# Optimization experiments

Hardware: AMD Instinct MI355X
Metric: run time of the kernel (lower is better)

## Reference

```python
import jax, jax.numpy as jnp
import numpy as np

EPS_MSG = 1e-7
EPS_BN = 1e-5


def _seg_softmax(logits, seg, num_segments):
    # logits: [E, D] per-edge logits; softmax over edges sharing the same dst node
    m = jax.ops.segment_max(logits, seg, num_segments=num_segments)
    m = jnp.where(jnp.isfinite(m), m, 0.0)
    e = jnp.exp(logits - m[seg])
    s = jax.ops.segment_sum(e, seg, num_segments=num_segments)
    return e / (s[seg] + 1e-16)


def _batchnorm(h, gamma, beta):
    mu = jnp.mean(h, axis=0)
    var = jnp.var(h, axis=0)
    return (h - mu) * jax.lax.rsqrt(var + EPS_BN) * gamma + beta


def setup_inputs() -> dict:
    key = jax.random.key(0)
    ks = jax.random.split(key, 12)
    N, E, G, D, L = 100000, 600000, 512, 128, 7
    x = jax.random.randint(ks[0], (N, 9), 0, 64, dtype=jnp.int32)
    edge_index = jax.random.randint(ks[1], (2, E), 0, N, dtype=jnp.int32)
    edge_attr = jax.random.randint(ks[2], (E, 3), 0, 8, dtype=jnp.int32)
    batch = jnp.sort(jax.random.randint(ks[3], (N,), 0, G, dtype=jnp.int32))
    rf_pred = jax.random.uniform(ks[4], (G,), dtype=jnp.float32)
    atom_emb = jax.random.normal(ks[5], (9, 64, D), dtype=jnp.float32) * 0.02
    bond_emb = jax.random.normal(ks[6], (3, 8, D), dtype=jnp.float32) * 0.02
    conv_w = jax.random.normal(ks[7], (L, D, D), dtype=jnp.float32) * 0.02
    conv_b = jnp.zeros((L, D), dtype=jnp.float32)
    ts = jnp.ones((L,), dtype=jnp.float32)  # learnable inverse temperatures (init 1/t style)
    gammas = jnp.ones((L, D), dtype=jnp.float32)
    bn_betas = jnp.zeros((L, D), dtype=jnp.float32)
    final_w = jax.random.normal(ks[8], (D, 1), dtype=jnp.float32) * 0.02
    final_b = jnp.zeros((1,), dtype=jnp.float32)
    beta = jnp.array([0.5], dtype=jnp.float32)
    return {"x": x, "edge_index": edge_index, "edge_attr": edge_attr, "batch": batch,
            "rf_pred": rf_pred, "atom_emb": atom_emb, "bond_emb": bond_emb,
            "conv_w": conv_w, "conv_b": conv_b, "ts": ts, "gammas": gammas,
            "bn_betas": bn_betas, "final_w": final_w, "final_b": final_b, "beta": beta}


def reference(x, edge_index, edge_attr, batch, rf_pred, atom_emb, bond_emb,
              conv_w, conv_b, ts, gammas, bn_betas, final_w, final_b, beta):
    N = x.shape[0]
    G = rf_pred.shape[0]
    L = conv_w.shape[0]
    src, dst = edge_index[0], edge_index[1]

    # AtomEncoder / BondEncoder: sum of per-feature embeddings
    h = jax.vmap(lambda tab, idx: tab[idx], in_axes=(0, 1))(atom_emb, x).sum(0)          # [N, D]
    e_emb = jax.vmap(lambda tab, idx: tab[idx], in_axes=(0, 1))(bond_emb, edge_attr).sum(0)  # [E, D]

    def genconv(l, hin):
        msg = jax.nn.relu(hin[src] + e_emb) + EPS_MSG          # [E, D]
        alpha = _seg_softmax(msg * ts[l], dst, N)              # softmax aggregation weights
        aggr = jax.ops.segment_sum(alpha * msg, dst, num_segments=N)  # [N, D]
        return (hin + aggr) @ conv_w[l] + conv_b[l]

    # res+ DeeperGCN
    h = genconv(0, h)
    for l in range(1, L):
        h2 = jax.nn.relu(_batchnorm(h, gammas[l - 1], bn_betas[l - 1]))
        h = genconv(l, h2) + h
    h = jax.nn.relu(_batchnorm(h, gammas[L - 1], bn_betas[L - 1]))

    # mean graph pooling
    counts = jnp.maximum(jax.ops.segment_sum(jnp.ones((N,), h.dtype), batch, num_segments=G), 1.0)
    hg = jax.ops.segment_sum(h, batch, num_segments=G) / counts[:, None]  # [G, D]

    dgcn_pred = hg @ final_w + final_b  # [G, 1]
    return (1.0 - beta) * jax.nn.sigmoid(dgcn_pred) + beta * rf_pred.reshape(-1, 1)
```

## Files before the change

kernel.cpp:

```cpp
#include <hip/hip_runtime.h>
#include <hip/hip_fp16.h>
#include <math.h>

#define D 128
#define PF 8

typedef _Float16 f16x8 __attribute__((ext_vector_type(8)));
typedef float f32x4_t __attribute__((ext_vector_type(4)));


__global__ void hist_kernel(const int* __restrict__ edge_index, int* __restrict__ deg, int E) {
    int e = blockIdx.x * blockDim.x + threadIdx.x;
    if (e >= E) return;
    atomicAdd(&deg[edge_index[E + e]], 1);
}

__global__ void scanA_kernel(const int* __restrict__ deg, int* __restrict__ bsum, int n) {
    __shared__ int red[256];
    int b = blockIdx.x, t = threadIdx.x;
    int base = b * 1024 + t * 4;
    int s = 0;
#pragma unroll
    for (int j = 0; j < 4; ++j)
        if (base + j < n) s += deg[base + j];
    red[t] = s;
    __syncthreads();
    for (int off = 128; off > 0; off >>= 1) {
        if (t < off) red[t] += red[t + off];
        __syncthreads();
    }
    if (t == 0) bsum[b] = red[0];
}

__global__ void scanB_kernel(int* __restrict__ bsum, int nb) {
    __shared__ int sh[256];
    int t = threadIdx.x;
    sh[t] = (t < nb) ? bsum[t] : 0;
    __syncthreads();
    for (int off = 1; off < 256; off <<= 1) {
        int v = (t >= off) ? sh[t - off] : 0;
        __syncthreads();
        sh[t] += v;
        __syncthreads();
    }
    if (t < nb) bsum[t] = (t == 0) ? 0 : sh[t - 1];
}

__global__ void scanC_kernel(const int* __restrict__ deg, const int* __restrict__ boff,
                             int* __restrict__ row_start, int n) {
    __shared__ int sh[256];
    int b = blockIdx.x, t = threadIdx.x;
    int base = b * 1024 + t * 4;
    int v[4];
#pragma unroll
    for (int j = 0; j < 4; ++j) v[j] = (base + j < n) ? deg[base + j] : 0;
    int p[4];
    p[0] = 0; p[1] = v[0]; p[2] = v[0] + v[1]; p[3] = v[0] + v[1] + v[2];
    int s = p[3] + v[3];
    sh[t] = s;
    __syncthreads();
    for (int off = 1; off < 256; off <<= 1) {
        int x = (t >= off) ? sh[t - off] : 0;
        __syncthreads();
        sh[t] += x;
        __syncthreads();
    }
    int off0 = boff[b] + sh[t] - s;
#pragma unroll
    for (int j = 0; j < 4; ++j)
        if (base + j < n) row_start[base + j] = off0 + p[j];
    if (base <= n - 1 && n - 1 < base + 4) row_start[n] = off0 + s;
}

__global__ void scatter_kernel(const int* __restrict__ edge_index, const int* __restrict__ edge_attr,
                               int* __restrict__ cursor, int2* __restrict__ csr, int E) {
    int e = blockIdx.x * blockDim.x + threadIdx.x;
    if (e >= E) return;
    int src = edge_index[e];
    int dst = edge_index[E + e];
    int pos = atomicAdd(&cursor[dst], 1);
    int a0 = edge_attr[e * 3], a1 = edge_attr[e * 3 + 1], a2 = edge_attr[e * 3 + 2];
    csr[pos] = make_int2(src, a0 | (a1 << 3) | (a2 << 6));
}

__global__ void ev_build_kernel(const float* __restrict__ bond_emb, __half2* __restrict__ evt) {
    int idx = blockIdx.x * blockDim.x + threadIdx.x;
    if (idx >= 512 * 64) return;
    int combo = idx >> 6, j = idx & 63;
    int d0 = 2 * j;
    float ex = bond_emb[(combo & 7) * D + d0] +
               bond_emb[(8 + ((combo >> 3) & 7)) * D + d0] +
               bond_emb[(16 + ((combo >> 6) & 7)) * D + d0];
    float ey = bond_emb[(combo & 7) * D + d0 + 1] +
               bond_emb[(8 + ((combo >> 3) & 7)) * D + d0 + 1] +
               bond_emb[(16 + ((combo >> 6) & 7)) * D + d0 + 1];
    evt[idx] = __floats2half2_rn(ex, ey);
}

__global__ void wt_build_kernel(const float* __restrict__ conv_w, _Float16* __restrict__ wt,
                                int total) {
    int idx = blockIdx.x * blockDim.x + threadIdx.x;
    if (idx >= total) return;
    int l = idx >> 14;
    int rem = idx & 16383;
    int n = rem >> 7, k = rem & 127;
    wt[idx] = (_Float16)conv_w[(l << 14) + k * 128 + n];
}

__global__ void gstart_kernel(const int* __restrict__ batch, int* __restrict__ gstart,
                              int N, int G) {
    int n = blockIdx.x * blockDim.x + threadIdx.x;
    if (n >= N) return;
    if (n == 0) {
        for (int g = 0; g <= batch[0]; ++g) gstart[g] = 0;
    } else {
        int b0 = batch[n - 1], b1 = batch[n];
        for (int g = b0 + 1; g <= b1; ++g) gstart[g] = n;
    }
    if (n == N - 1) {
        for (int g = batch[N - 1] + 1; g <= G; ++g) gstart[g] = N;
    }
}


__global__ void atom_embed_kernel(const int* __restrict__ x,
                                  const float* __restrict__ atom_emb,
                                  _Float16* __restrict__ h16, int N) {
    long long idx = (long long)blockIdx.x * blockDim.x + threadIdx.x;
    if (idx >= (long long)N * D) return;
    int n = (int)(idx >> 7);
    int d = (int)(idx & 127);
    float acc = 0.f;
#pragma unroll
    for (int f = 0; f < 9; ++f) {
        int v = x[n * 9 + f];
        acc += atom_emb[(long long)(f * 64 + v) * D + d];
    }
    h16[idx] = (_Float16)acc;
}

__global__ void bn_reduce_finalize_kernel(const float* __restrict__ partial, int nb,
                                          const float* __restrict__ gamma,
                                          const float* __restrict__ bnbeta, float invN,
                                          float* __restrict__ aArr, float* __restrict__ bArr) {
    __shared__ float r1[256], r2[256];
    int d = blockIdx.x, t = threadIdx.x;
    float a1 = 0.f, a2 = 0.f;
    for (int i = t; i < nb; i += 256) {
        a1 += partial[(long long)i * 256 + d];
        a2 += partial[(long long)i * 256 + 128 + d];
    }
    r1[t] = a1; r2[t] = a2;
    __syncthreads();
    for (int off = 128; off > 0; off >>= 1) {
        if (t < off) { r1[t] += r1[t + off]; r2[t] += r2[t + off]; }
        __syncthreads();
    }
    if (t == 0) {
        float mean = r1[0] * invN;
        float var = r2[0] * invN - mean * mean;
        float a = rsqrtf(var + 1e-5f) * gamma[d];
        aArr[d] = a;
        bArr[d] = bnbeta[d] - mean * a;
    }
}

__global__ __launch_bounds__(128, 8) void fused_layer_kernel(
        const __half2* __restrict__ h16c,
        const float* __restrict__ aArr, const float* __restrict__ bArr, int applyBN,
        const float* __restrict__ ts, int l,
        const int* __restrict__ row_start, const int2* __restrict__ csr,
        const __half2* __restrict__ evt,
        const _Float16* __restrict__ wt, const float* __restrict__ bias,
        int residual, _Float16* __restrict__ h16out,
        float* __restrict__ partial, int N) {
    __shared__ __align__(16) char smem[8192];
    _Float16* yh = (_Float16*)smem;
    __half2* tile = (__half2*)smem;

    int t = threadIdx.x;
    int row0 = blockIdx.x * 16;
    int wave = t >> 6;
    int lane = t & 63;
    float tsl = ts[l];
    int a = row0 + wave * 8;

    float2 bnA = make_float2(1.f, 0.f), bnB = make_float2(0.f, 0.f);
    if (applyBN) {
        bnA = ((const float2*)aArr)[lane];
        bnB = ((const float2*)bArr)[lane];
    }

    int rsv = row_start[min(a + min(lane, 8), N)];
    int s0 = __builtin_amdgcn_readlane(rsv, 0);
    int s1 = __builtin_amdgcn_readlane(rsv, 8);

#pragma unroll
    for (int i = 0; i < 8; ++i) {
        int r = a + i;
        float2 hs = make_float2(0.f, 0.f);
        if (r < N) {
            hs = __half22float2(h16c[(size_t)r * 64 + lane]);
            if (applyBN) {
                hs.x = fmaxf(hs.x * bnA.x + bnB.x, 0.f);
                hs.y = fmaxf(hs.y * bnA.y + bnB.y, 0.f);
            }
        }
        tile[(wave * 8 + i) * 68 + lane] = __floats2half2_rn(hs.x, hs.y);
    }

    int c0 = s0;
    int2 ea = make_int2(0, 0);
    if (c0 + lane < s1) ea = csr[c0 + lane];

    __half2 hvS[PF], evS[PF];
#pragma unroll
    for (int k = 0; k < PF; ++k) {
        int pp = s0 + k;
        if (pp < s1) {
            int q = pp - c0;
            int srcp = __builtin_amdgcn_readlane(ea.x, q);
            int cbp = __builtin_amdgcn_readlane(ea.y, q);
            hvS[k] = h16c[(size_t)srcp * 64 + lane];
            evS[k] = evt[(size_t)cbp * 64 + lane];
        }
    }

    int cur = 0;
    int nend = __builtin_amdgcn_readlane(rsv, min(cur + 1, 8));
    while (cur < 8 && nend == s0) {
        cur++;
        nend = __builtin_amdgcn_readlane(rsv, min(cur + 1, 8));
    }

    float accwx = 0.f, accwy = 0.f, accmx = 0.f, accmy = 0.f;
    int total = s1 - s0;
    for (int it = 0; it < total; it += PF) {
#pragma unroll
        for (int k = 0; k < PF; ++k) {
            int p = s0 + it + k;
            if (p < s1) {
                float2 hv = __half22float2(hvS[k]);
                float2 ev = __half22float2(evS[k]);
                if (applyBN) {
                    hv.x = fmaxf(hv.x * bnA.x + bnB.x, 0.f);
                    hv.y = fmaxf(hv.y * bnA.y + bnB.y, 0.f);
                }
                float mx = fmaxf(hv.x + ev.x, 0.f) + 1e-7f;
                float my = fmaxf(hv.y + ev.y, 0.f) + 1e-7f;
                float wx = __expf(mx * tsl);
                float wy = __expf(my * tsl);
                accwx += wx; accmx += wx * mx;
                accwy += wy; accmy += wy * my;
                int pp = p + PF;
                if (pp < s1) {
                    if (pp >= c0 + 64) {
                        c0 += 64;
                        ea = (c0 + lane < s1) ? csr[c0 + lane] : make_int2(0, 0);
                    }
                    int q = pp - c0;
                    int srcp = __builtin_amdgcn_readlane(ea.x, q);
                    int cbp = __builtin_amdgcn_readlane(ea.y, q);
                    hvS[k] = h16c[(size_t)srcp * 64 + lane];
                    evS[k] = evt[(size_t)cbp * 64 + lane];
                }
                while (cur < 8 && nend == p + 1) {
                    int slot = (wave * 8 + cur) * 68 + lane;
                    float2 y = __half22float2(tile[slot]);
                    y.x += accmx / (accwx + 1e-16f);
                    y.y += accmy / (accwy + 1e-16f);
                    tile[slot] = __floats2half2_rn(y.x, y.y);
                    accwx = accwy = accmx = accmy = 0.f;
                    cur++;
                    nend = __builtin_amdgcn_readlane(rsv, min(cur + 1, 8));
                }
            }
        }
    }
    __syncthreads();

    int ln = t & 15;
    int quad = (t & 63) >> 4;
    const _Float16* h16in = (const _Float16*)h16c;

    float cs[4] = {0.f, 0.f, 0.f, 0.f};
    float cq[4] = {0.f, 0.f, 0.f, 0.f};
    const _Float16* ap = yh + ln * 136 + quad * 8;
#pragma unroll
    for (int ct = 0; ct < 4; ++ct) {
        int colg = (wave * 4 + ct) * 16 + ln;
        const _Float16* bp = wt + (size_t)colg * 128 + quad * 8;
        f32x4_t c = {0.f, 0.f, 0.f, 0.f};
#pragma unroll
        for (int kk = 0; kk < 4; ++kk) {
            f16x8 av = *(const f16x8*)(ap + kk * 32);
            f16x8 bv = *(const f16x8*)(bp + kk * 32);
            c = __builtin_amdgcn_mfma_f32_16x16x32_f16(av, bv, c, 0, 0, 0);
        }
        float bsv = bias[colg];
#pragma unroll
        for (int reg = 0; reg < 4; ++reg) {
            int r = row0 + quad * 4 + reg;
            if (r < N) {
                long long off = (long long)r * D + colg;
                float o = c[reg] + bsv;
                if (residual) o += (float)h16in[off];
                h16out[off] = (_Float16)o;
                cs[ct] += o; cq[ct] += o * o;
            }
        }
    }

    __syncthreads();
    float* stats = (float*)smem;
    int grp = wave * 4 + quad;
#pragma unroll
    for (int ct = 0; ct < 4; ++ct) {
        int colg = (wave * 4 + ct) * 16 + ln;
        stats[grp * 256 + colg] = cs[ct];
        stats[grp * 256 + 128 + colg] = cq[ct];
    }
    __syncthreads();
    float ssumA = 0.f, ssumB = 0.f;
#pragma unroll
    for (int g = 0; g < 8; ++g) {
        ssumA += stats[g * 256 + t];
        ssumB += stats[g * 256 + 128 + t];
    }
    partial[(long long)blockIdx.x * 256 + t] = ssumA;
    partial[(long long)blockIdx.x * 256 + 128 + t] = ssumB;
}

__global__ void pool_head_kernel(const _Float16* __restrict__ h16, const float* __restrict__ aArr,
                                 const float* __restrict__ bArr, const int* __restrict__ gstart,
                                 const float* __restrict__ fw, const float* __restrict__ fb,
                                 const float* __restrict__ beta, const float* __restrict__ rf,
                                 float* __restrict__ out) {
    __shared__ float red[256];
    int g = blockIdx.x, t = threadIdx.x;
    int d = t & 127, half = t >> 7;
    int s0 = gstart[g], s1 = gstart[g + 1];
    float a = aArr[d], b = bArr[d];
    float acc = 0.f;
    for (int n = s0 + half; n < s1; n += 2)
        acc += fmaxf((float)h16[(long long)n * D + d] * a + b, 0.f);
    red[t] = acc;
    __syncthreads();
    if (t < 128) red[t] += red[t + 128];
    __syncthreads();
    if (t < 64) {
        float v = red[t] * fw[t] + red[t + 64] * fw[t + 64];
#pragma unroll
        for (int off = 32; off > 0; off >>= 1) v += __shfl_down(v, off);
        if (t == 0) {
            float c = fmaxf((float)(s1 - s0), 1.f);
            float pred = v / c + fb[0];
            float sig = 1.f / (1.f + __expf(-pred));
            float bb = beta[0];
            out[g] = (1.f - bb) * sig + bb * rf[g];
        }
    }
}

static inline size_t align16(size_t x) { return (x + 15) & ~(size_t)15; }

extern "C" void kernel_launch(void* const* d_in, const int* in_sizes, int n_in,
                              void* d_out, int out_size, void* d_ws, size_t ws_size,
                              hipStream_t stream) {
    const int* x = (const int*)d_in[0];
    const int* edge_index = (const int*)d_in[1];
    const int* edge_attr = (const int*)d_in[2];
    const int* batch = (const int*)d_in[3];
    const float* rf_pred = (const float*)d_in[4];
    const float* atom_emb = (const float*)d_in[5];
    const float* bond_emb = (const float*)d_in[6];
    const float* conv_w = (const float*)d_in[7];
    const float* conv_b = (const float*)d_in[8];
    const float* ts = (const float*)d_in[9];
    const float* gammas = (const float*)d_in[10];
    const float* bn_betas = (const float*)d_in[11];
    const float* final_w = (const float*)d_in[12];
    const float* final_b = (const float*)d_in[13];
    const float* beta = (const float*)d_in[14];
    float* out = (float*)d_out;

    int N = in_sizes[0] / 9;
    int E = in_sizes[1] / 2;
    int G = in_sizes[4];
    int L = in_sizes[9];

    int mmBlocks = (N + 15) / 16;
    size_t ND = (size_t)N * D;

    char* p = (char*)d_ws;
    _Float16* h16_a = (_Float16*)p;  p += align16(ND * 2);
    _Float16* h16_b = (_Float16*)p;  p += align16(ND * 2);
    __half2* evt = (__half2*)p;      p += align16((size_t)512 * 64 * 4);
    _Float16* wt = (_Float16*)p;     p += align16((size_t)L * 16384 * 2);
    float* partial = (float*)p;      p += align16((size_t)256 * mmBlocks * 4);
    float* aArr = (float*)p;         p += align16((size_t)D * 4);
    float* bArr = (float*)p;         p += align16((size_t)D * 4);
    int* gstart = (int*)p;           p += align16((size_t)(G + 1) * 4);
    int* deg = (int*)p;              p += align16((size_t)N * 4);
    int* row_start = (int*)p;        p += align16((size_t)(N + 1) * 4);
    int* cursor = (int*)p;           p += align16((size_t)N * 4);
    int* bsum = (int*)p;             p += align16((size_t)256 * 4);
    int2* csr = (int2*)p;            p += align16((size_t)E * 8);

    long long ndThreads = (long long)N * D;
    int ndBlocks = (int)((ndThreads + 255) / 256);
    int eBlocks = (E + 255) / 256;
    int nBlocks = (N + 255) / 256;
    int nb1024 = (N + 1023) / 1024;
    int wtTotal = L * 16384;
    float invN = 1.0f / (float)N;

    hipMemsetAsync(deg, 0, (size_t)N * sizeof(int), stream);
    hist_kernel<<<eBlocks, 256, 0, stream>>>(edge_index, deg, E);
    scanA_kernel<<<nb1024, 256, 0, stream>>>(deg, bsum, N);
    scanB_kernel<<<1, 256, 0, stream>>>(bsum, nb1024);
    scanC_kernel<<<nb1024, 256, 0, stream>>>(deg, bsum, row_start, N);
    hipMemcpyAsync(cursor, row_start, (size_t)N * sizeof(int), hipMemcpyDeviceToDevice, stream);
    scatter_kernel<<<eBlocks, 256, 0, stream>>>(edge_index, edge_attr, cursor, csr, E);
    ev_build_kernel<<<(512 * 64 + 255) / 256, 256, 0, stream>>>(bond_emb, evt);
    wt_build_kernel<<<(wtTotal + 255) / 256, 256, 0, stream>>>(conv_w, wt, wtTotal);
    gstart_kernel<<<nBlocks, 256, 0, stream>>>(batch, gstart, N, G);

    atom_embed_kernel<<<ndBlocks, 256, 0, stream>>>(x, atom_emb, h16_a, N);

    _Float16* h16c = h16_a;
    _Float16* h16n = h16_b;
    for (int l = 0; l < L; ++l) {
        int applyBN = (l >= 1) ? 1 : 0;
        if (applyBN) {
            bn_reduce_finalize_kernel<<<128, 256, 0, stream>>>(
                partial, mmBlocks, gammas + (size_t)(l - 1) * D,
                bn_betas + (size_t)(l - 1) * D, invN, aArr, bArr);
        }
        fused_layer_kernel<<<mmBlocks, 128, 0, stream>>>(
            (const __half2*)h16c, aArr, bArr, applyBN, ts, l, row_start, csr, evt,
            wt + (size_t)l * 16384, conv_b + (size_t)l * D,
            applyBN, h16n, partial, N);
        _Float16* tmp16 = h16c; h16c = h16n; h16n = tmp16;
    }

    bn_reduce_finalize_kernel<<<128, 256, 0, stream>>>(
        partial, mmBlocks, gammas + (size_t)(L - 1) * D,
        bn_betas + (size_t)(L - 1) * D, invN, aArr, bArr);
    pool_head_kernel<<<G, 256, 0, stream>>>(h16c, aArr, bArr, gstart,
                                            final_w, final_b, beta, rf_pred, out);
}
```

Baseline: 917.8 us.

## Fuse setup kernels, prefetch CSR chunk, raise gather prefetch depth, register self rows

Merges the three small setup kernels into one launch and writes the cursor array inside the scan kernel instead of a separate device copy. In the fused layer kernel, self-row features are kept in registers and written to the LDS tile once per row close, avoiding a read-modify-write of the tile. The next 64-edge CSR chunk is now loaded ahead of time, and the gather prefetch depth goes from 8 to 12. This trades extra VGPR pressure, and possibly lower occupancy, for more memory-level parallelism.

```diff
diff --git a/kernel.cpp b/kernel.cpp
--- a/kernel.cpp
+++ b/kernel.cpp
@@ -3,7 +3,7 @@
 #include <math.h>
 
 #define D 128
-#define PF 8
+#define PF 12
 
 typedef _Float16 f16x8 __attribute__((ext_vector_type(8)));
 typedef float f32x4_t __attribute__((ext_vector_type(4)));
@@ -47,7 +47,7 @@
 }
 
 __global__ void scanC_kernel(const int* __restrict__ deg, const int* __restrict__ boff,
-                             int* __restrict__ row_start, int n) {
+                             int* __restrict__ row_start, int* __restrict__ cursor, int n) {
     __shared__ int sh[256];
     int b = blockIdx.x, t = threadIdx.x;
     int base = b * 1024 + t * 4;
@@ -68,7 +68,10 @@
     int off0 = boff[b] + sh[t] - s;
 #pragma unroll
     for (int j = 0; j < 4; ++j)
-        if (base + j < n) row_start[base + j] = off0 + p[j];
+        if (base + j < n) {
+            row_start[base + j] = off0 + p[j];
+            cursor[base + j] = off0 + p[j];
+        }
     if (base <= n - 1 && n - 1 < base + 4) row_start[n] = off0 + s;
 }
 
@@ -83,33 +86,32 @@
     csr[pos] = make_int2(src, a0 | (a1 << 3) | (a2 << 6));
 }
 
-__global__ void ev_build_kernel(const float* __restrict__ bond_emb, __half2* __restrict__ evt) {
+__global__ void misc_build_kernel(const float* __restrict__ bond_emb, __half2* __restrict__ evt,
+                                  const float* __restrict__ conv_w, _Float16* __restrict__ wt,
+                                  int wtTotal, const int* __restrict__ batch,
+                                  int* __restrict__ gstart, int N, int G) {
     int idx = blockIdx.x * blockDim.x + threadIdx.x;
-    if (idx >= 512 * 64) return;
-    int combo = idx >> 6, j = idx & 63;
-    int d0 = 2 * j;
-    float ex = bond_emb[(combo & 7) * D + d0] +
-               bond_emb[(8 + ((combo >> 3) & 7)) * D + d0] +
-               bond_emb[(16 + ((combo >> 6) & 7)) * D + d0];
-    float ey = bond_emb[(combo & 7) * D + d0 + 1] +
-               bond_emb[(8 + ((combo >> 3) & 7)) * D + d0 + 1] +
-               bond_emb[(16 + ((combo >> 6) & 7)) * D + d0 + 1];
-    evt[idx] = __floats2half2_rn(ex, ey);
-}
-
-__global__ void wt_build_kernel(const float* __restrict__ conv_w, _Float16* __restrict__ wt,
-                                int total) {
-    int idx = blockIdx.x * blockDim.x + threadIdx.x;
-    if (idx >= total) return;
-    int l = idx >> 14;
-    int rem = idx & 16383;
-    int n = rem >> 7, k = rem & 127;
-    wt[idx] = (_Float16)conv_w[(l << 14) + k * 128 + n];
-}
-
-__global__ void gstart_kernel(const int* __restrict__ batch, int* __restrict__ gstart,
-                              int N, int G) {
-    int n = blockIdx.x * blockDim.x + threadIdx.x;
+    if (idx < 512 * 64) {
+        int combo = idx >> 6, j = idx & 63;
+        int d0 = 2 * j;
+        float ex = bond_emb[(combo & 7) * D + d0] +
+                   bond_emb[(8 + ((combo >> 3) & 7)) * D + d0] +
+                   bond_emb[(16 + ((combo >> 6) & 7)) * D + d0];
+        float ey = bond_emb[(combo & 7) * D + d0 + 1] +
+                   bond_emb[(8 + ((combo >> 3) & 7)) * D + d0 + 1] +
+                   bond_emb[(16 + ((combo >> 6) & 7)) * D + d0 + 1];
+        evt[idx] = __floats2half2_rn(ex, ey);
+        return;
+    }
+    int widx = idx - 512 * 64;
+    if (widx < wtTotal) {
+        int l = widx >> 14;
+        int rem = widx & 16383;
+        int n = rem >> 7, k = rem & 127;
+        wt[widx] = (_Float16)conv_w[(l << 14) + k * 128 + n];
+        return;
+    }
+    int n = widx - wtTotal;
     if (n >= N) return;
     if (n == 0) {
         for (int g = 0; g <= batch[0]; ++g) gstart[g] = 0;
@@ -192,48 +194,71 @@
     }
 
     int rsv = row_start[min(a + min(lane, 8), N)];
+    __half2 zero2 = __floats2half2_rn(0.f, 0.f);
+    __half2 hsv0 = zero2, hsv1 = zero2, hsv2 = zero2, hsv3 = zero2;
+    __half2 hsv4 = zero2, hsv5 = zero2, hsv6 = zero2, hsv7 = zero2;
+    if (a + 0 < N) hsv0 = h16c[(size_t)(a + 0) * 64 + lane];
+    if (a + 1 < N) hsv1 = h16c[(size_t)(a + 1) * 64 + lane];
+    if (a + 2 < N) hsv2 = h16c[(size_t)(a + 2) * 64 + lane];
+    if (a + 3 < N) hsv3 = h16c[(size_t)(a + 3) * 64 + lane];
+    if (a + 4 < N) hsv4 = h16c[(size_t)(a + 4) * 64 + lane];
+    if (a + 5 < N) hsv5 = h16c[(size_t)(a + 5) * 64 + lane];
+    if (a + 6 < N) hsv6 = h16c[(size_t)(a + 6) * 64 + lane];
+    if (a + 7 < N) hsv7 = h16c[(size_t)(a + 7) * 64 + lane];
+
     int s0 = __builtin_amdgcn_readlane(rsv, 0);
     int s1 = __builtin_amdgcn_readlane(rsv, 8);
 
-#pragma unroll
-    for (int i = 0; i < 8; ++i) {
-        int r = a + i;
-        float2 hs = make_float2(0.f, 0.f);
-        if (r < N) {
-            hs = __half22float2(h16c[(size_t)r * 64 + lane]);
-            if (applyBN) {
-                hs.x = fmaxf(hs.x * bnA.x + bnB.x, 0.f);
-                hs.y = fmaxf(hs.y * bnA.y + bnB.y, 0.f);
-            }
-        }
-        tile[(wave * 8 + i) * 68 + lane] = __floats2half2_rn(hs.x, hs.y);
-    }
-
     int c0 = s0;
-    int2 ea = make_int2(0, 0);
-    if (c0 + lane < s1) ea = csr[c0 + lane];
+    int2 eaCur = make_int2(0, 0), eaNxt = make_int2(0, 0);
+    if (c0 + lane < s1) eaCur = csr[c0 + lane];
+    if (c0 + 64 + lane < s1) eaNxt = csr[c0 + 64 + lane];
 
     __half2 hvS[PF], evS[PF];
 #pragma unroll
     for (int k = 0; k < PF; ++k) {
         int pp = s0 + k;
         if (pp < s1) {
-            int q = pp - c0;
-            int srcp = __builtin_amdgcn_readlane(ea.x, q);
-            int cbp = __builtin_amdgcn_readlane(ea.y, q);
+            int srcp = __builtin_amdgcn_readlane(eaCur.x, k);
+            int cbp = __builtin_amdgcn_readlane(eaCur.y, k);
             hvS[k] = h16c[(size_t)srcp * 64 + lane];
             evS[k] = evt[(size_t)cbp * 64 + lane];
         }
     }
 
+    float accwx = 0.f, accwy = 0.f, accmx = 0.f, accmy = 0.f;
     int cur = 0;
-    int nend = __builtin_amdgcn_readlane(rsv, min(cur + 1, 8));
-    while (cur < 8 && nend == s0) {
-        cur++;
-        nend = __builtin_amdgcn_readlane(rsv, min(cur + 1, 8));
-    }
-
-    float accwx = 0.f, accwy = 0.f, accmx = 0.f, accmy = 0.f;
+    int nend = __builtin_amdgcn_readlane(rsv, 1);
+
+#define CLOSE_ROW()                                                          \
+    {                                                                        \
+        __half2 hh;                                                          \
+        switch (cur) {                                                       \
+            case 0: hh = hsv0; break;                                        \
+            case 1: hh = hsv1; break;                                        \
+            case 2: hh = hsv2; break;                                        \
+            case 3: hh = hsv3; break;                                        \
+            case 4: hh = hsv4; break;                                        \
+            case 5: hh = hsv5; break;                                        \
+            case 6: hh = hsv6; break;                                        \
+            default: hh = hsv7; break;                                       \
+        }                                                                    \
+        float2 hs2 = __half22float2(hh);                                     \
+        if (applyBN) {                                                       \
+            hs2.x = fmaxf(hs2.x * bnA.x + bnB.x, 0.f);                       \
+            hs2.y = fmaxf(hs2.y * bnA.y + bnB.y, 0.f);                       \
+        }                                                                    \
+        float2 yy;                                                           \
+        yy.x = hs2.x + accmx / (accwx + 1e-16f);                             \
+        yy.y = hs2.y + accmy / (accwy + 1e-16f);                             \
+        tile[(wave * 8 + cur) * 68 + lane] = __floats2half2_rn(yy.x, yy.y);  \
+        accwx = accwy = accmx = accmy = 0.f;                                 \
+        cur++;                                                               \
+        nend = __builtin_amdgcn_readlane(rsv, min(cur + 1, 8));              \
+    }
+
+    while (cur < 8 && nend == s0) CLOSE_ROW();
+
     int total = s1 - s0;
     for (int it = 0; it < total; it += PF) {
 #pragma unroll
@@ -256,27 +281,21 @@
                 if (pp < s1) {
                     if (pp >= c0 + 64) {
                         c0 += 64;
-                        ea = (c0 + lane < s1) ? csr[c0 + lane] : make_int2(0, 0);
+                        eaCur = eaNxt;
+                        eaNxt = make_int2(0, 0);
+                        if (c0 + 64 + lane < s1) eaNxt = csr[c0 + 64 + lane];
                     }
                     int q = pp - c0;
-                    int srcp = __builtin_amdgcn_readlane(ea.x, q);
-                    int cbp = __builtin_amdgcn_readlane(ea.y, q);
+                    int srcp = __builtin_amdgcn_readlane(eaCur.x, q);
+                    int cbp = __builtin_amdgcn_readlane(eaCur.y, q);
                     hvS[k] = h16c[(size_t)srcp * 64 + lane];
                     evS[k] = evt[(size_t)cbp * 64 + lane];
                 }
-                while (cur < 8 && nend == p + 1) {
-                    int slot = (wave * 8 + cur) * 68 + lane;
-                    float2 y = __half22float2(tile[slot]);
-                    y.x += accmx / (accwx + 1e-16f);
-                    y.y += accmy / (accwy + 1e-16f);
-                    tile[slot] = __floats2half2_rn(y.x, y.y);
-                    accwx = accwy = accmx = accmy = 0.f;
-                    cur++;
-                    nend = __builtin_amdgcn_readlane(rsv, min(cur + 1, 8));
-                }
+                while (cur < 8 && nend == p + 1) CLOSE_ROW();
             }
         }
     }
+#undef CLOSE_ROW
     __syncthreads();
 
     int ln = t & 15;
@@ -389,7 +408,7 @@
     int G = in_sizes[4];
     int L = in_sizes[9];
 
-    int mmBlocks = (N + 15) / 16;
+    int nTiles = (N + 15) / 16;
     size_t ND = (size_t)N * D;
 
     char* p = (char*)d_ws;
@@ -397,7 +416,7 @@
     _Float16* h16_b = (_Float16*)p;  p += align16(ND * 2);
     __half2* evt = (__half2*)p;      p += align16((size_t)512 * 64 * 4);
     _Float16* wt = (_Float16*)p;     p += align16((size_t)L * 16384 * 2);
-    float* partial = (float*)p;      p += align16((size_t)256 * mmBlocks * 4);
+    float* partial = (float*)p;      p += align16((size_t)256 * nTiles * 4);
     float* aArr = (float*)p;         p += align16((size_t)D * 4);
     float* bArr = (float*)p;         p += align16((size_t)D * 4);
     int* gstart = (int*)p;           p += align16((size_t)(G + 1) * 4);
@@ -410,21 +429,20 @@
     long long ndThreads = (long long)N * D;
     int ndBlocks = (int)((ndThreads + 255) / 256);
     int eBlocks = (E + 255) / 256;
-    int nBlocks = (N + 255) / 256;
     int nb1024 = (N + 1023) / 1024;
     int wtTotal = L * 16384;
+    int miscTotal = 512 * 64 + wtTotal + N;
+    int miscBlocks = (miscTotal + 255) / 256;
     float invN = 1.0f / (float)N;
 
     hipMemsetAsync(deg, 0, (size_t)N * sizeof(int), stream);
     hist_kernel<<<eBlocks, 256, 0, stream>>>(edge_index, deg, E);
     scanA_kernel<<<nb1024, 256, 0, stream>>>(deg, bsum, N);
     scanB_kernel<<<1, 256, 0, stream>>>(bsum, nb1024);
-    scanC_kernel<<<nb1024, 256, 0, stream>>>(deg, bsum, row_start, N);
-    hipMemcpyAsync(cursor, row_start, (size_t)N * sizeof(int), hipMemcpyDeviceToDevice, stream);
+    scanC_kernel<<<nb1024, 256, 0, stream>>>(deg, bsum, row_start, cursor, N);
     scatter_kernel<<<eBlocks, 256, 0, stream>>>(edge_index, edge_attr, cursor, csr, E);
-    ev_build_kernel<<<(512 * 64 + 255) / 256, 256, 0, stream>>>(bond_emb, evt);
-    wt_build_kernel<<<(wtTotal + 255) / 256, 256, 0, stream>>>(conv_w, wt, wtTotal);
-    gstart_kernel<<<nBlocks, 256, 0, stream>>>(batch, gstart, N, G);
+    misc_build_kernel<<<miscBlocks, 256, 0, stream>>>(bond_emb, evt, conv_w, wt, wtTotal,
+                                                      batch, gstart, N, G);
 
     atom_embed_kernel<<<ndBlocks, 256, 0, stream>>>(x, atom_emb, h16_a, N);
 
@@ -434,10 +452,10 @@
         int applyBN = (l >= 1) ? 1 : 0;
         if (applyBN) {
             bn_reduce_finalize_kernel<<<128, 256, 0, stream>>>(
-                partial, mmBlocks, gammas + (size_t)(l - 1) * D,
+                partial, nTiles, gammas + (size_t)(l - 1) * D,
                 bn_betas + (size_t)(l - 1) * D, invN, aArr, bArr);
         }
-        fused_layer_kernel<<<mmBlocks, 128, 0, stream>>>(
+        fused_layer_kernel<<<nTiles, 128, 0, stream>>>(
             (const __half2*)h16c, aArr, bArr, applyBN, ts, l, row_start, csr, evt,
             wt + (size_t)l * 16384, conv_b + (size_t)l * D,
             applyBN, h16n, partial, N);
@@ -445,7 +463,7 @@
     }
 
     bn_reduce_finalize_kernel<<<128, 256, 0, stream>>>(
-        partial, mmBlocks, gammas + (size_t)(L - 1) * D,
+        partial, nTiles, gammas + (size_t)(L - 1) * D,
         bn_betas + (size_t)(L - 1) * D, invN, aArr, bArr);
     pool_head_kernel<<<G, 256, 0, stream>>>(h16c, aArr, bArr, gstart,
                                             final_w, final_b, beta, rf_pred, out);
```

Result: faster. 880.5 us (-4.1%).
